# Optimization experiments

Hardware: AMD Instinct MI355X
Metric: run time of the kernel (lower is better)

Reference implementation:

```python
import jax, jax.numpy as jnp
import numpy as np

E = 64      # hidden_dim
FF = 128    # ff_dim
H = 4       # nhead
D = E // H  # head_dim = 16
STEPS = 16  # recursion_steps
IN = 200    # input_dim
B = 131072  # batch


def _ln(h, g, b):
    m = h.mean(-1, keepdims=True)
    v = ((h - m) ** 2).mean(-1, keepdims=True)
    return (h - m) * jax.lax.rsqrt(v + 1e-5) * g + b


def _ffn(h, w1, b1, w2, b2):
    return jax.nn.gelu(h @ w1.T + b1, approximate=False) @ w2.T + b2


def _forward(x, W_in, b_in, g_in, be_in,
             z_in_w, z_in_b, z_out_w, z_out_b,
             z_ffn_w1, z_ffn_b1, z_ffn_w2, z_ffn_b2,
             zn1_g, zn1_b, zn2_g, zn2_b,
             y_in_w, y_in_b, y_out_w, y_out_b,
             y_ffn_w1, y_ffn_b1, y_ffn_w2, y_ffn_b2,
             yn1_g, yn1_b, yn2_g, yn2_b,
             W_out, b_out):
    Bn = x.shape[0]
    x_proj = jax.nn.gelu(_ln(x @ W_in.T + b_in, g_in, be_in), approximate=False)  # [B,E]
    y0 = jnp.zeros((Bn, E), dtype=x.dtype)
    z0 = jnp.zeros((Bn, E), dtype=x.dtype)
    scale = 1.0 / np.sqrt(D).astype(np.float32)
    Wv_y = y_in_w[2 * E:]   # cross-attn over a single kv token: softmax weight == 1,
    bv_y = y_in_b[2 * E:]   # so output = out_proj(v_proj(z)) exactly (no approximation)

    def step(carry, _):
        y, z = carry
        seq = jnp.stack([x_proj, y, z], axis=1)            # [B,3,E]
        qkv = seq @ z_in_w.T + z_in_b                      # [B,3,3E]
        q, k, v = jnp.split(qkv, 3, axis=-1)
        rh = lambda t: t.reshape(Bn, 3, H, D).transpose(0, 2, 1, 3)  # [B,H,3,D]
        q, k, v = rh(q), rh(k), rh(v)
        att = jax.nn.softmax(jnp.einsum('bhsd,bhtd->bhst', q, k) * scale, axis=-1)
        o = jnp.einsum('bhst,bhtd->bhsd', att, v).transpose(0, 2, 1, 3).reshape(Bn, 3, E)
        o = o @ z_out_w.T + z_out_b
        z_res = _ln(z + o[:, 2, :], zn1_g, zn1_b)
        z2 = _ln(z_res + _ffn(z_res, z_ffn_w1, z_ffn_b1, z_ffn_w2, z_ffn_b2), zn2_g, zn2_b)
        ca = (z2 @ Wv_y.T + bv_y) @ y_out_w.T + y_out_b    # 1-token cross-attention
        y_res = _ln(y + ca, yn1_g, yn1_b)
        y2 = _ln(y_res + _ffn(y_res, y_ffn_w1, y_ffn_b1, y_ffn_w2, y_ffn_b2), yn2_g, yn2_b)
        return (y2, z2), None

    (y, z), _ = jax.lax.scan(step, (y0, z0), None, length=STEPS)
    return (y @ W_out.T + b_out)[:, 0]                     # [B]


def setup_inputs() -> dict:
    key = jax.random.key(0)
    ks = jax.random.split(key, 12)
    f = lambda k, s: jax.random.normal(k, s, dtype=jnp.float32) * 0.05
    zeros = lambda s: jnp.zeros(s, dtype=jnp.float32)
    ones = lambda s: jnp.ones(s, dtype=jnp.float32)
    return {
        'x': jax.random.normal(ks[0], (B, IN), dtype=jnp.float32),
        'W_in': f(ks[1], (E, IN)), 'b_in': zeros((E,)),
        'g_in': ones((E,)), 'be_in': zeros((E,)),
        'z_in_w': f(ks[2], (3 * E, E)), 'z_in_b': zeros((3 * E,)),
        'z_out_w': f(ks[3], (E, E)), 'z_out_b': zeros((E,)),
        'z_ffn_w1': f(ks[4], (FF, E)), 'z_ffn_b1': zeros((FF,)),
        'z_ffn_w2': f(ks[5], (E, FF)), 'z_ffn_b2': zeros((E,)),
        'zn1_g': ones((E,)), 'zn1_b': zeros((E,)),
        'zn2_g': ones((E,)), 'zn2_b': zeros((E,)),
        'y_in_w': f(ks[6], (3 * E, E)), 'y_in_b': zeros((3 * E,)),
        'y_out_w': f(ks[7], (E, E)), 'y_out_b': zeros((E,)),
        'y_ffn_w1': f(ks[8], (FF, E)), 'y_ffn_b1': zeros((FF,)),
        'y_ffn_w2': f(ks[9], (E, FF)), 'y_ffn_b2': zeros((E,)),
        'yn1_g': ones((E,)), 'yn1_b': zeros((E,)),
        'yn2_g': ones((E,)), 'yn2_b': zeros((E,)),
        'W_out': f(ks[10], (1, E)), 'b_out': zeros((1,)),
    }


def reference(x, W_in, b_in, g_in, be_in,
              z_in_w, z_in_b, z_out_w, z_out_b,
              z_ffn_w1, z_ffn_b1, z_ffn_w2, z_ffn_b2,
              zn1_g, zn1_b, zn2_g, zn2_b,
              y_in_w, y_in_b, y_out_w, y_out_b,
              y_ffn_w1, y_ffn_b1, y_ffn_w2, y_ffn_b2,
              yn1_g, yn1_b, yn2_g, yn2_b,
              W_out, b_out):
    return _forward(x, W_in, b_in, g_in, be_in,
                    z_in_w, z_in_b, z_out_w, z_out_b,
                    z_ffn_w1, z_ffn_b1, z_ffn_w2, z_ffn_b2,
                    zn1_g, zn1_b, zn2_g, zn2_b,
                    y_in_w, y_in_b, y_out_w, y_out_b,
                    y_ffn_w1, y_ffn_b1, y_ffn_w2, y_ffn_b2,
                    yn1_g, yn1_b, yn2_g, yn2_b,
                    W_out, b_out)
```

## Files before the change

### kernel.cpp

```cpp
#include <hip/hip_runtime.h>
#include <math.h>


constexpr int STEPS = 16;
constexpr int INDIM = 200;

typedef __attribute__((ext_vector_type(8))) short bfrag8;
typedef __attribute__((ext_vector_type(4))) float f32x4;
typedef __attribute__((ext_vector_type(4))) short s16x4;

constexpr int FB_WIN  = 0;
constexpr int NFRAG   = 140;
constexpr int NPARAM  = 1544;

constexpr int LB_ZQ   = 0;
constexpr int LB_ZK   = 8;
constexpr int LB_ZV   = 16;
constexpr int LB_ZOUT = 24;
constexpr int LB_ZF1  = 32;
constexpr int LB_ZF2  = 48;
constexpr int LB_YV   = 64;
constexpr int LB_YOUT = 72;
constexpr int LB_YF1  = 80;
constexpr int LB_YF2  = 96;
constexpr int NSTEADY = 112;

constexpr int PB_BIN   = 0;
constexpr int PB_GIN   = 64;
constexpr int PB_BEIN  = 128;
constexpr int PB_ZINB  = 192;
constexpr int PB_ZOUTB = 384;
constexpr int PB_ZF1B  = 448;
constexpr int PB_ZF2B  = 576;
constexpr int PB_ZN1G  = 640;
constexpr int PB_ZN1B  = 704;
constexpr int PB_ZN2G  = 768;
constexpr int PB_ZN2B  = 832;
constexpr int PB_YVB   = 896;
constexpr int PB_YOUTB = 960;
constexpr int PB_YF1B  = 1024;
constexpr int PB_YF2B  = 1152;
constexpr int PB_YN1G  = 1216;
constexpr int PB_YN1B  = 1280;
constexpr int PB_YN2G  = 1344;
constexpr int PB_YN2B  = 1408;
constexpr int PB_WOUT  = 1472;
constexpr int PB_BOUT  = 1536;

constexpr int S64      = 72;
constexpr int L_W      = 0;
constexpr int L_P      = 57344;
constexpr int L_ACT    = 60432;
constexpr int WAVE_SH  = 1152;
constexpr int NWAVE    = 16;
constexpr int ARENA_SH = L_ACT + NWAVE * WAVE_SH;

struct Params {
  const float *x, *W_in, *b_in, *g_in, *be_in;
  const float *z_in_w, *z_in_b, *z_out_w, *z_out_b;
  const float *z_ffn_w1, *z_ffn_b1, *z_ffn_w2, *z_ffn_b2;
  const float *zn1_g, *zn1_b, *zn2_g, *zn2_b;
  const float *y_in_w, *y_in_b, *y_out_w, *y_out_b;
  const float *y_ffn_w1, *y_ffn_b1, *y_ffn_w2, *y_ffn_b2;
  const float *yn1_g, *yn1_b, *yn2_g, *yn2_b;
  const float *W_out, *b_out;
  float *out;
  int nrows;
};

__device__ __forceinline__ ushort f2bf_rne(float f) {
  uint u = __float_as_uint(f);
  u += 0x7FFFu + ((u >> 16) & 1u);
  return (ushort)(u >> 16);
}

__device__ __forceinline__ ushort f2bf(float f) {
  return (ushort)((__float_as_uint(f) + 0x8000u) >> 16);
}
__device__ __forceinline__ uint pk2(float a, float b) {
  uint ua = __float_as_uint(a) + 0x8000u;
  uint ub = __float_as_uint(b) + 0x8000u;
  return (ua >> 16) | (ub & 0xFFFF0000u);
}
__device__ __forceinline__ float upk_lo(uint u) {
  return __uint_as_float(u << 16);
}
__device__ __forceinline__ float upk_hi(uint u) {
  return __uint_as_float(u & 0xFFFF0000u);
}
__device__ __forceinline__ f32x4 upk4(const uint* p) {
  f32x4 r;
  r.x = upk_lo(p[0]); r.y = upk_hi(p[0]);
  r.z = upk_lo(p[1]); r.w = upk_hi(p[1]);
  return r;
}
__device__ __forceinline__ float dot4(f32x4 a, f32x4 b) {
  return a.x * b.x + a.y * b.y + a.z * b.z + a.w * b.w;
}
__device__ __forceinline__ void stc(short* buf, int stride, int mt, int q,
                                    int s, f32x4 c) {
  s16x4 v;
  v.x = (short)f2bf(c.x); v.y = (short)f2bf(c.y);
  v.z = (short)f2bf(c.z); v.w = (short)f2bf(c.w);
  *(s16x4*)(buf + s * stride + mt * 16 + q * 4) = v;
}

__device__ __forceinline__ void c2b_p(const uint p[8], bfrag8& b0, bfrag8& b1,
                                      int lane) {
  const int srcA = (lane & 15) | ((lane & 16) << 1);
  const int srcB = srcA + 16;
  const bool odd = (lane & 32) != 0;
  uint ev0 = p[0], ev1 = p[1], ev2 = p[4], ev3 = p[5];
  uint od0 = p[2], od1 = p[3], od2 = p[6], od3 = p[7];
  uint rA0, rA1, rA2, rA3, rB0, rB1, rB2, rB3;
  {
    uint e, o;
    e = (uint)__shfl((int)ev0, srcA); o = (uint)__shfl((int)od0, srcA); rA0 = odd ? o : e;
    e = (uint)__shfl((int)ev1, srcA); o = (uint)__shfl((int)od1, srcA); rA1 = odd ? o : e;
    e = (uint)__shfl((int)ev2, srcA); o = (uint)__shfl((int)od2, srcA); rA2 = odd ? o : e;
    e = (uint)__shfl((int)ev3, srcA); o = (uint)__shfl((int)od3, srcA); rA3 = odd ? o : e;
    e = (uint)__shfl((int)ev0, srcB); o = (uint)__shfl((int)od0, srcB); rB0 = odd ? o : e;
    e = (uint)__shfl((int)ev1, srcB); o = (uint)__shfl((int)od1, srcB); rB1 = odd ? o : e;
    e = (uint)__shfl((int)ev2, srcB); o = (uint)__shfl((int)od2, srcB); rB2 = odd ? o : e;
    e = (uint)__shfl((int)ev3, srcB); o = (uint)__shfl((int)od3, srcB); rB3 = odd ? o : e;
  }
  union U { uint u[4]; bfrag8 b; };
  U u0, u1;
  u0.u[0] = rA0; u0.u[1] = rA1; u0.u[2] = rB0; u0.u[3] = rB1;
  u1.u[0] = rA2; u1.u[1] = rA3; u1.u[2] = rB2; u1.u[3] = rB3;
  b0 = u0.b; b1 = u1.b;
}
__device__ __forceinline__ void c2b(const f32x4 c[4], bfrag8& b0, bfrag8& b1,
                                    int lane) {
  uint p[8];
#pragma unroll
  for (int mt = 0; mt < 4; ++mt) {
    p[2 * mt]     = pk2(c[mt].x, c[mt].y);
    p[2 * mt + 1] = pk2(c[mt].z, c[mt].w);
  }
  c2b_p(p, b0, b1, lane);
}

template <int MT>
__device__ __forceinline__ void layerN(const short* in, const short* lw,
                                       int fbase, const float* bias, f32x4* c,
                                       int lane, int q, int s) {
  bfrag8 bf[2];
#pragma unroll
  for (int kt = 0; kt < 2; ++kt)
    bf[kt] = *(const bfrag8*)(in + s * S64 + kt * 32 + q * 8);
#pragma unroll
  for (int mt = 0; mt < MT; ++mt)
    c[mt] = *(const f32x4*)(bias + mt * 16 + q * 4);
#pragma unroll
  for (int mt = 0; mt < MT; ++mt) {
#pragma unroll
    for (int kt = 0; kt < 2; ++kt) {
      bfrag8 af = *(const bfrag8*)(lw + (fbase + mt * 2 + kt) * 512 + lane * 8);
      c[mt] = __builtin_amdgcn_mfma_f32_16x16x32_bf16(af, bf[kt], c[mt], 0, 0, 0);
    }
  }
}

template <int MT, int KT>
__device__ __forceinline__ void layerBK(const bfrag8* bf, const short* lw,
                                        int fbase, const float* bias, f32x4* c,
                                        int lane, int q) {
#pragma unroll
  for (int mt = 0; mt < MT; ++mt)
    c[mt] = *(const f32x4*)(bias + mt * 16 + q * 4);
#pragma unroll
  for (int mt = 0; mt < MT; ++mt) {
#pragma unroll
    for (int kt = 0; kt < KT; ++kt) {
      bfrag8 af = *(const bfrag8*)(lw + (fbase + mt * KT + kt) * 512 + lane * 8);
      c[mt] = __builtin_amdgcn_mfma_f32_16x16x32_bf16(af, bf[kt], c[mt], 0, 0, 0);
    }
  }
}

template <int MT>
__device__ __forceinline__ void layerB2(const bfrag8* bfA, const bfrag8* bfB,
                                        const short* lw, int fbase,
                                        const float* bias, f32x4* cA, f32x4* cB,
                                        int lane, int q) {
#pragma unroll
  for (int mt = 0; mt < MT; ++mt) {
    f32x4 b4 = *(const f32x4*)(bias + mt * 16 + q * 4);
    cA[mt] = b4; cB[mt] = b4;
  }
#pragma unroll
  for (int mt = 0; mt < MT; ++mt) {
#pragma unroll
    for (int kt = 0; kt < 2; ++kt) {
      bfrag8 af = *(const bfrag8*)(lw + (fbase + mt * 2 + kt) * 512 + lane * 8);
      cA[mt] = __builtin_amdgcn_mfma_f32_16x16x32_bf16(af, bfA[kt], cA[mt], 0, 0, 0);
      cB[mt] = __builtin_amdgcn_mfma_f32_16x16x32_bf16(af, bfB[kt], cB[mt], 0, 0, 0);
    }
  }
}

__device__ __forceinline__ void ffn2_via_th(const f32x4 h8[8], short* TH,
                                            const short* lw, int f2base,
                                            const float* b2, f32x4 c[4],
                                            int lane, int q, int s);

__device__ __forceinline__ void lnorm_c(f32x4 c[4], const float* g,
                                        const float* b, int q) {
  f32x4 s4 = (c[0] + c[1]) + (c[2] + c[3]);
  float sm = (s4.x + s4.y) + (s4.z + s4.w);
  sm += __shfl_xor(sm, 16); sm += __shfl_xor(sm, 32);
  float mean = sm * (1.f / 64.f);
  f32x4 vs4 = {0.f, 0.f, 0.f, 0.f};
#pragma unroll
  for (int mt = 0; mt < 4; ++mt) {
    f32x4 d = c[mt] - mean;
    c[mt] = d;
    vs4 = vs4 + d * d;
  }
  float vs = (vs4.x + vs4.y) + (vs4.z + vs4.w);
  vs += __shfl_xor(vs, 16); vs += __shfl_xor(vs, 32);
  float rs = rsqrtf(vs * (1.f / 64.f) + 1e-5f);
#pragma unroll
  for (int mt = 0; mt < 4; ++mt) {
    f32x4 g4 = *(const f32x4*)(g + mt * 16 + q * 4);
    f32x4 b4 = *(const f32x4*)(b + mt * 16 + q * 4);
    c[mt] = (c[mt] * rs) * g4 + b4;
  }
}

__device__ __forceinline__ f32x4 gelu4(f32x4 x) {
  const float K = 0.70710678118654752f;
  f32x4 ax;
  ax.x = fabsf(x.x) * K; ax.y = fabsf(x.y) * K;
  ax.z = fabsf(x.z) * K; ax.w = fabsf(x.w) * K;
  f32x4 u = ax * 0.47047f + 1.0f;
  f32x4 t;
  t.x = __builtin_amdgcn_rcpf(u.x); t.y = __builtin_amdgcn_rcpf(u.y);
  t.z = __builtin_amdgcn_rcpf(u.z); t.w = __builtin_amdgcn_rcpf(u.w);
  f32x4 poly = ((t * 0.7478556f + (-0.0958798f)) * t + 0.3480242f) * t;
  f32x4 gq = ax * ax;
  f32x4 e;
  e.x = __expf(-gq.x); e.y = __expf(-gq.y);
  e.z = __expf(-gq.z); e.w = __expf(-gq.w);
  f32x4 r = poly * e;
  f32x4 er;
  er.x = copysignf(1.0f - r.x, x.x); er.y = copysignf(1.0f - r.y, x.y);
  er.z = copysignf(1.0f - r.z, x.z); er.w = copysignf(1.0f - r.w, x.w);
  f32x4 h = x * 0.5f;
  return h + h * er;
}

__device__ __forceinline__ void ffn2_via_th(const f32x4 h8[8], short* TH,
                                            const short* lw, int f2base,
                                            const float* b2, f32x4 c[4],
                                            int lane, int q, int s) {
#pragma unroll
  for (int mt = 0; mt < 4; ++mt)
    c[mt] = *(const f32x4*)(b2 + mt * 16 + q * 4);
#pragma unroll
  for (int g = 0; g < 2; ++g) {
#pragma unroll
    for (int mt = 0; mt < 4; ++mt)
      stc(TH, S64, mt, q, s, gelu4(h8[4 * g + mt]));
    bfrag8 bf[2];
#pragma unroll
    for (int kt = 0; kt < 2; ++kt)
      bf[kt] = *(const bfrag8*)(TH + s * S64 + kt * 32 + q * 8);
#pragma unroll
    for (int mt = 0; mt < 4; ++mt) {
#pragma unroll
      for (int kt = 0; kt < 2; ++kt) {
        bfrag8 af =
            *(const bfrag8*)(lw + (f2base + mt * 4 + 2 * g + kt) * 512 + lane * 8);
        c[mt] = __builtin_amdgcn_mfma_f32_16x16x32_bf16(af, bf[kt], c[mt], 0, 0, 0);
      }
    }
  }
}

__global__ void prepack_kernel(Params p, ushort* wf) {
  int f = blockIdx.x;
  int lane = threadIdx.x;

  if (f == NFRAG) {
    float* pw = (float*)(wf + (size_t)NFRAG * 512);
    for (int t = lane; t < NPARAM; t += 64) {
      float v = 0.f;
      if      (t < 64)   v = p.b_in[t];
      else if (t < 128)  v = p.g_in[t - 64];
      else if (t < 192)  v = p.be_in[t - 128];
      else if (t < 384)  v = p.z_in_b[t - 192];
      else if (t < 448)  v = p.z_out_b[t - 384];
      else if (t < 576)  v = p.z_ffn_b1[t - 448];
      else if (t < 640)  v = p.z_ffn_b2[t - 576];
      else if (t < 704)  v = p.zn1_g[t - 640];
      else if (t < 768)  v = p.zn1_b[t - 704];
      else if (t < 832)  v = p.zn2_g[t - 768];
      else if (t < 896)  v = p.zn2_b[t - 832];
      else if (t < 960)  v = p.y_in_b[128 + t - 896];
      else if (t < 1024) v = p.y_out_b[t - 960];
      else if (t < 1152) v = p.y_ffn_b1[t - 1024];
      else if (t < 1216) v = p.y_ffn_b2[t - 1152];
      else if (t < 1280) v = p.yn1_g[t - 1216];
      else if (t < 1344) v = p.yn1_b[t - 1280];
      else if (t < 1408) v = p.yn2_g[t - 1344];
      else if (t < 1472) v = p.yn2_b[t - 1408];
      else if (t < 1536) v = p.W_out[t - 1472];
      else if (t == 1536) v = p.b_out[0];
      pw[t] = v;
    }
    return;
  }

  int q = lane >> 4, r = lane & 15;
  const float* src; int K, mt, kt, l;
  if (f < 28)        { src = p.W_in;                K = 200; mt = f / 7;  kt = f % 7; }
  else if (f < 36)   { l = f - 28;  src = p.z_in_w;            K = 64;  mt = l / 2; kt = l % 2; }
  else if (f < 44)   { l = f - 36;  src = p.z_in_w + 64 * 64;  K = 64;  mt = l / 2; kt = l % 2; }
  else if (f < 52)   { l = f - 44;  src = p.z_in_w + 128 * 64; K = 64;  mt = l / 2; kt = l % 2; }
  else if (f < 60)   { l = f - 52;  src = p.z_out_w;           K = 64;  mt = l / 2; kt = l % 2; }
  else if (f < 76)   { l = f - 60;  src = p.z_ffn_w1;          K = 64;  mt = l / 2; kt = l % 2; }
  else if (f < 92)   { l = f - 76;  src = p.z_ffn_w2;          K = 128; mt = l / 4; kt = l % 4; }
  else if (f < 100)  { l = f - 92;  src = p.y_in_w + 128 * 64; K = 64;  mt = l / 2; kt = l % 2; }
  else if (f < 108)  { l = f - 100; src = p.y_out_w;           K = 64;  mt = l / 2; kt = l % 2; }
  else if (f < 124)  { l = f - 108; src = p.y_ffn_w1;          K = 64;  mt = l / 2; kt = l % 2; }
  else               { l = f - 124; src = p.y_ffn_w2;          K = 128; mt = l / 4; kt = l % 4; }

  int row = mt * 16 + r;
  int col = kt * 32 + q * 8;
  bfrag8 o;
#pragma unroll
  for (int j = 0; j < 8; ++j) {
    int cc = col + j;
    float v = (cc < K) ? src[(size_t)row * K + cc] : 0.0f;
    o[j] = (short)f2bf_rne(v);
  }
  *(bfrag8*)(wf + (size_t)f * 512 + lane * 8) = o;
}

__global__ __launch_bounds__(1024, 1)
void trm_mfma_kernel(Params p, const ushort* wf) {
  __shared__ __align__(16) short arena[ARENA_SH];
  const int tid = threadIdx.x;
  const int wave = tid >> 6, lane = tid & 63;
  const int q = lane >> 4, s = lane & 15;

  {
    const uint4* srcw = (const uint4*)(wf + (size_t)28 * 512);
    uint4* dstw = (uint4*)(arena + L_W);
    for (int i = tid; i < NSTEADY * 64; i += 1024) dstw[i] = srcw[i];
    const uint4* srcp = (const uint4*)(wf + (size_t)NFRAG * 512);
    uint4* dstp = (uint4*)(arena + L_P);
    for (int i = tid; i < NPARAM / 4; i += 1024) dstp[i] = srcp[i];
  }
  __syncthreads();

  const short* LW = arena + L_W;
  const float* P  = (const float*)(arena + L_P);
  short* TH = arena + L_ACT + wave * WAVE_SH;

  const int chunks = (p.nrows + 255) / 256;
  for (int ic = blockIdx.x; ic < chunks; ic += gridDim.x) {
    const int row0 = ic * 256 + wave * 16;
    int row = row0 + s;
    if (row >= p.nrows) row = p.nrows - 1;

    bfrag8 xpB[2];
    {
      const float* xr = p.x + (size_t)row * INDIM;
      bfrag8 xb[7];
#pragma unroll
      for (int kt = 0; kt < 7; ++kt) {
        int k0i = kt * 32 + q * 8;
        bfrag8 t;
        if (kt < 6 || q == 0) {
          f32x4 lo = *(const f32x4*)(xr + k0i);
          f32x4 hi = *(const f32x4*)(xr + k0i + 4);
          t[0] = (short)f2bf(lo.x); t[1] = (short)f2bf(lo.y);
          t[2] = (short)f2bf(lo.z); t[3] = (short)f2bf(lo.w);
          t[4] = (short)f2bf(hi.x); t[5] = (short)f2bf(hi.y);
          t[6] = (short)f2bf(hi.z); t[7] = (short)f2bf(hi.w);
        } else {
#pragma unroll
          for (int j = 0; j < 8; ++j) t[j] = 0;
        }
        xb[kt] = t;
      }
      f32x4 c[4];
#pragma unroll
      for (int mt = 0; mt < 4; ++mt)
        c[mt] = *(const f32x4*)(P + PB_BIN + mt * 16 + q * 4);
#pragma unroll
      for (int mt = 0; mt < 4; ++mt)
#pragma unroll
        for (int kt = 0; kt < 7; ++kt) {
          bfrag8 af =
              *(const bfrag8*)(wf + (size_t)(FB_WIN + mt * 7 + kt) * 512 + lane * 8);
          c[mt] = __builtin_amdgcn_mfma_f32_16x16x32_bf16(af, xb[kt], c[mt], 0, 0, 0);
        }
      lnorm_c(c, P + PB_GIN, P + PB_BEIN, q);
#pragma unroll
      for (int mt = 0; mt < 4; ++mt) c[mt] = gelu4(c[mt]);
      c2b(c, xpB[0], xpB[1], lane);
    }

    uint k0p[8], v0p[8], zCp[8], yCp[8];
    bfrag8 zB[2], yB[2];
    {
      f32x4 ck[4], cv[4];
      layerBK<4, 2>(xpB, LW, LB_ZK, P + PB_ZINB + 64, ck, lane, q);
      layerBK<4, 2>(xpB, LW, LB_ZV, P + PB_ZINB + 128, cv, lane, q);
#pragma unroll
      for (int mt = 0; mt < 4; ++mt) {
        k0p[2 * mt]     = pk2(ck[mt].x, ck[mt].y);
        k0p[2 * mt + 1] = pk2(ck[mt].z, ck[mt].w);
        v0p[2 * mt]     = pk2(cv[mt].x, cv[mt].y);
        v0p[2 * mt + 1] = pk2(cv[mt].z, cv[mt].w);
        zCp[2 * mt] = 0u; zCp[2 * mt + 1] = 0u;
        yCp[2 * mt] = 0u; yCp[2 * mt + 1] = 0u;
      }
#pragma unroll
      for (int kt = 0; kt < 2; ++kt) {
        bfrag8 t;
#pragma unroll
        for (int j = 0; j < 8; ++j) t[j] = 0;
        zB[kt] = t; yB[kt] = t;
      }
    }

    for (int st = 0; st < STEPS; ++st) {
      float w0[4], w1[4], w2[4], wi[4];
      {
        f32x4 q2[4], kz[4], ky[4];
        layerBK<4, 2>(zB, LW, LB_ZQ, P + PB_ZINB, q2, lane, q);
        layerB2<4>(zB, yB, LW, LB_ZK, P + PB_ZINB + 64, kz, ky, lane, q);
#pragma unroll
        for (int mt = 0; mt < 4; ++mt) {
          float a0 = dot4(q2[mt], upk4(k0p + 2 * mt));
          float a1 = dot4(q2[mt], ky[mt]);
          float a2 = dot4(q2[mt], kz[mt]);
          a0 += __shfl_xor(a0, 16); a0 += __shfl_xor(a0, 32);
          a1 += __shfl_xor(a1, 16); a1 += __shfl_xor(a1, 32);
          a2 += __shfl_xor(a2, 16); a2 += __shfl_xor(a2, 32);
          a0 *= 0.25f; a1 *= 0.25f; a2 *= 0.25f;
          float mx = fmaxf(a0, fmaxf(a1, a2));
          float e0 = __expf(a0 - mx), e1 = __expf(a1 - mx), e2 = __expf(a2 - mx);
          w0[mt] = e0; w1[mt] = e1; w2[mt] = e2;
          wi[mt] = __builtin_amdgcn_rcpf(e0 + e1 + e2);
        }
      }
      {
        f32x4 vz[4], vy[4];
        layerB2<4>(zB, yB, LW, LB_ZV, P + PB_ZINB + 128, vz, vy, lane, q);
#pragma unroll
        for (int mt = 0; mt < 4; ++mt) {
          f32x4 v0 = upk4(v0p + 2 * mt);
          f32x4 o = (v0 * w0[mt] + vy[mt] * w1[mt] + vz[mt] * w2[mt]) * wi[mt];
          stc(TH, S64, mt, q, s, o);
        }
      }

      uint zrp[8];
      {
        f32x4 zr[4];
        layerN<4>(TH, LW, LB_ZOUT, P + PB_ZOUTB, zr, lane, q, s);
#pragma unroll
        for (int mt = 0; mt < 4; ++mt) zr[mt] = zr[mt] + upk4(zCp + 2 * mt);
        lnorm_c(zr, P + PB_ZN1G, P + PB_ZN1B, q);
#pragma unroll
        for (int mt = 0; mt < 4; ++mt) {
          stc(TH, S64, mt, q, s, zr[mt]);
          zrp[2 * mt]     = pk2(zr[mt].x, zr[mt].y);
          zrp[2 * mt + 1] = pk2(zr[mt].z, zr[mt].w);
        }
      }

      f32x4 z2[4];
      {
        f32x4 h8[8];
        layerN<8>(TH, LW, LB_ZF1, P + PB_ZF1B, h8, lane, q, s);
        ffn2_via_th(h8, TH, LW, LB_ZF2, P + PB_ZF2B, z2, lane, q, s);
      }
#pragma unroll
      for (int mt = 0; mt < 4; ++mt) z2[mt] = z2[mt] + upk4(zrp + 2 * mt);
      lnorm_c(z2, P + PB_ZN2G, P + PB_ZN2B, q);
      {
        uint zp[8];
#pragma unroll
        for (int mt = 0; mt < 4; ++mt) {
          zp[2 * mt]     = pk2(z2[mt].x, z2[mt].y);
          zp[2 * mt + 1] = pk2(z2[mt].z, z2[mt].w);
          zCp[2 * mt] = zp[2 * mt]; zCp[2 * mt + 1] = zp[2 * mt + 1];
        }
        c2b_p(zp, zB[0], zB[1], lane);
      }

      f32x4 t4[4];
      layerBK<4, 2>(zB, LW, LB_YV, P + PB_YVB, t4, lane, q);
#pragma unroll
      for (int mt = 0; mt < 4; ++mt) stc(TH, S64, mt, q, s, t4[mt]);

      uint yrp[8];
      {
        f32x4 yr[4];
        layerN<4>(TH, LW, LB_YOUT, P + PB_YOUTB, yr, lane, q, s);
#pragma unroll
        for (int mt = 0; mt < 4; ++mt) yr[mt] = yr[mt] + upk4(yCp + 2 * mt);
        lnorm_c(yr, P + PB_YN1G, P + PB_YN1B, q);
#pragma unroll
        for (int mt = 0; mt < 4; ++mt) {
          stc(TH, S64, mt, q, s, yr[mt]);
          yrp[2 * mt]     = pk2(yr[mt].x, yr[mt].y);
          yrp[2 * mt + 1] = pk2(yr[mt].z, yr[mt].w);
        }
      }

      f32x4 y2[4];
      {
        f32x4 h8[8];
        layerN<8>(TH, LW, LB_YF1, P + PB_YF1B, h8, lane, q, s);
        ffn2_via_th(h8, TH, LW, LB_YF2, P + PB_YF2B, y2, lane, q, s);
      }
#pragma unroll
      for (int mt = 0; mt < 4; ++mt) y2[mt] = y2[mt] + upk4(yrp + 2 * mt);
      lnorm_c(y2, P + PB_YN2G, P + PB_YN2B, q);
      {
        uint yp[8];
#pragma unroll
        for (int mt = 0; mt < 4; ++mt) {
          yp[2 * mt]     = pk2(y2[mt].x, y2[mt].y);
          yp[2 * mt + 1] = pk2(y2[mt].z, y2[mt].w);
          yCp[2 * mt] = yp[2 * mt]; yCp[2 * mt + 1] = yp[2 * mt + 1];
        }
        c2b_p(yp, yB[0], yB[1], lane);
      }
    }

    float acc = 0.f;
#pragma unroll
    for (int mt = 0; mt < 4; ++mt) {
      f32x4 w4 = *(const f32x4*)(P + PB_WOUT + mt * 16 + q * 4);
      acc += dot4(upk4(yCp + 2 * mt), w4);
    }
    acc += __shfl_xor(acc, 16); acc += __shfl_xor(acc, 32);
    if (q == 0 && (row0 + s) < p.nrows) p.out[row0 + s] = acc + P[PB_BOUT];
  }
}

extern "C" void kernel_launch(void* const* d_in, const int* in_sizes, int n_in,
                              void* d_out, int out_size, void* d_ws,
                              size_t ws_size, hipStream_t stream) {
  Params p;
  const float* const* in = (const float* const*)d_in;
  p.x        = in[0];  p.W_in     = in[1];  p.b_in     = in[2];
  p.g_in     = in[3];  p.be_in    = in[4];
  p.z_in_w   = in[5];  p.z_in_b   = in[6];
  p.z_out_w  = in[7];  p.z_out_b  = in[8];
  p.z_ffn_w1 = in[9];  p.z_ffn_b1 = in[10];
  p.z_ffn_w2 = in[11]; p.z_ffn_b2 = in[12];
  p.zn1_g    = in[13]; p.zn1_b    = in[14];
  p.zn2_g    = in[15]; p.zn2_b    = in[16];
  p.y_in_w   = in[17]; p.y_in_b   = in[18];
  p.y_out_w  = in[19]; p.y_out_b  = in[20];
  p.y_ffn_w1 = in[21]; p.y_ffn_b1 = in[22];
  p.y_ffn_w2 = in[23]; p.y_ffn_b2 = in[24];
  p.yn1_g    = in[25]; p.yn1_b    = in[26];
  p.yn2_g    = in[27]; p.yn2_b    = in[28];
  p.W_out    = in[29]; p.b_out    = in[30];
  p.out      = (float*)d_out;
  p.nrows    = in_sizes[0] / INDIM;

  if (ws_size < (size_t)NFRAG * 1024 + NPARAM * 4) return;
  ushort* wf = (ushort*)d_ws;

  hipLaunchKernelGGL(prepack_kernel, dim3(NFRAG + 1), dim3(64), 0, stream, p, wf);
  hipLaunchKernelGGL(trm_mfma_kernel, dim3(256), dim3(1024), 0, stream, p, wf);
}
```

Measured before the change: 838.3 us.

## Process two 16-row tiles per wave to reuse weight fragments across MFMAs

```diff
diff --git a/kernel.cpp b/kernel.cpp
--- a/kernel.cpp
+++ b/kernel.cpp
@@ -142,39 +142,28 @@
 }
 
 template <int MT>
-__device__ __forceinline__ void layerN(const short* in, const short* lw,
-                                       int fbase, const float* bias, f32x4* c,
-                                       int lane, int q, int s) {
-  bfrag8 bf[2];
-#pragma unroll
-  for (int kt = 0; kt < 2; ++kt)
-    bf[kt] = *(const bfrag8*)(in + s * S64 + kt * 32 + q * 8);
-#pragma unroll
-  for (int mt = 0; mt < MT; ++mt)
-    c[mt] = *(const f32x4*)(bias + mt * 16 + q * 4);
+__device__ __forceinline__ void layerN2(const short* in0, const short* in1,
+                                        const short* lw, int fbase,
+                                        const float* bias, f32x4* c0, f32x4* c1,
+                                        int lane, int q, int s) {
+  bfrag8 b0[2], b1[2];
+#pragma unroll
+  for (int kt = 0; kt < 2; ++kt) {
+    b0[kt] = *(const bfrag8*)(in0 + s * S64 + kt * 32 + q * 8);
+    b1[kt] = *(const bfrag8*)(in1 + s * S64 + kt * 32 + q * 8);
+  }
+#pragma unroll
+  for (int mt = 0; mt < MT; ++mt) {
+    f32x4 b4 = *(const f32x4*)(bias + mt * 16 + q * 4);
+    c0[mt] = b4; c1[mt] = b4;
+  }
 #pragma unroll
   for (int mt = 0; mt < MT; ++mt) {
 #pragma unroll
     for (int kt = 0; kt < 2; ++kt) {
       bfrag8 af = *(const bfrag8*)(lw + (fbase + mt * 2 + kt) * 512 + lane * 8);
-      c[mt] = __builtin_amdgcn_mfma_f32_16x16x32_bf16(af, bf[kt], c[mt], 0, 0, 0);
-    }
-  }
-}
-
-template <int MT, int KT>
-__device__ __forceinline__ void layerBK(const bfrag8* bf, const short* lw,
-                                        int fbase, const float* bias, f32x4* c,
-                                        int lane, int q) {
-#pragma unroll
-  for (int mt = 0; mt < MT; ++mt)
-    c[mt] = *(const f32x4*)(bias + mt * 16 + q * 4);
-#pragma unroll
-  for (int mt = 0; mt < MT; ++mt) {
-#pragma unroll
-    for (int kt = 0; kt < KT; ++kt) {
-      bfrag8 af = *(const bfrag8*)(lw + (fbase + mt * KT + kt) * 512 + lane * 8);
-      c[mt] = __builtin_amdgcn_mfma_f32_16x16x32_bf16(af, bf[kt], c[mt], 0, 0, 0);
+      c0[mt] = __builtin_amdgcn_mfma_f32_16x16x32_bf16(af, b0[kt], c0[mt], 0, 0, 0);
+      c1[mt] = __builtin_amdgcn_mfma_f32_16x16x32_bf16(af, b1[kt], c1[mt], 0, 0, 0);
     }
   }
 }
@@ -200,10 +189,29 @@
   }
 }
 
-__device__ __forceinline__ void ffn2_via_th(const f32x4 h8[8], short* TH,
-                                            const short* lw, int f2base,
-                                            const float* b2, f32x4 c[4],
-                                            int lane, int q, int s);
+template <int MT>
+__device__ __forceinline__ void layerB4(const bfrag8* bf0, const bfrag8* bf1,
+                                        const bfrag8* bf2, const bfrag8* bf3,
+                                        const short* lw, int fbase,
+                                        const float* bias, f32x4* c0, f32x4* c1,
+                                        f32x4* c2, f32x4* c3, int lane, int q) {
+#pragma unroll
+  for (int mt = 0; mt < MT; ++mt) {
+    f32x4 b4 = *(const f32x4*)(bias + mt * 16 + q * 4);
+    c0[mt] = b4; c1[mt] = b4; c2[mt] = b4; c3[mt] = b4;
+  }
+#pragma unroll
+  for (int mt = 0; mt < MT; ++mt) {
+#pragma unroll
+    for (int kt = 0; kt < 2; ++kt) {
+      bfrag8 af = *(const bfrag8*)(lw + (fbase + mt * 2 + kt) * 512 + lane * 8);
+      c0[mt] = __builtin_amdgcn_mfma_f32_16x16x32_bf16(af, bf0[kt], c0[mt], 0, 0, 0);
+      c1[mt] = __builtin_amdgcn_mfma_f32_16x16x32_bf16(af, bf1[kt], c1[mt], 0, 0, 0);
+      c2[mt] = __builtin_amdgcn_mfma_f32_16x16x32_bf16(af, bf2[kt], c2[mt], 0, 0, 0);
+      c3[mt] = __builtin_amdgcn_mfma_f32_16x16x32_bf16(af, bf3[kt], c3[mt], 0, 0, 0);
+    }
+  }
+}
 
 __device__ __forceinline__ void lnorm_c(f32x4 c[4], const float* g,
                                         const float* b, int q) {
@@ -251,29 +259,37 @@
   return h + h * er;
 }
 
-__device__ __forceinline__ void ffn2_via_th(const f32x4 h8[8], short* TH,
-                                            const short* lw, int f2base,
-                                            const float* b2, f32x4 c[4],
-                                            int lane, int q, int s) {
-#pragma unroll
-  for (int mt = 0; mt < 4; ++mt)
-    c[mt] = *(const f32x4*)(b2 + mt * 16 + q * 4);
+__device__ __forceinline__ void ffn2_via_th2(const f32x4 h0[8], const f32x4 h1[8],
+                                             short* TH0, short* TH1,
+                                             const short* lw, int f2base,
+                                             const float* b2, f32x4 c0[4],
+                                             f32x4 c1[4], int lane, int q, int s) {
+#pragma unroll
+  for (int mt = 0; mt < 4; ++mt) {
+    f32x4 b4 = *(const f32x4*)(b2 + mt * 16 + q * 4);
+    c0[mt] = b4; c1[mt] = b4;
+  }
 #pragma unroll
   for (int g = 0; g < 2; ++g) {
 #pragma unroll
-    for (int mt = 0; mt < 4; ++mt)
-      stc(TH, S64, mt, q, s, gelu4(h8[4 * g + mt]));
-    bfrag8 bf[2];
-#pragma unroll
-    for (int kt = 0; kt < 2; ++kt)
-      bf[kt] = *(const bfrag8*)(TH + s * S64 + kt * 32 + q * 8);
+    for (int mt = 0; mt < 4; ++mt) {
+      stc(TH0, S64, mt, q, s, gelu4(h0[4 * g + mt]));
+      stc(TH1, S64, mt, q, s, gelu4(h1[4 * g + mt]));
+    }
+    bfrag8 bf0[2], bf1[2];
+#pragma unroll
+    for (int kt = 0; kt < 2; ++kt) {
+      bf0[kt] = *(const bfrag8*)(TH0 + s * S64 + kt * 32 + q * 8);
+      bf1[kt] = *(const bfrag8*)(TH1 + s * S64 + kt * 32 + q * 8);
+    }
 #pragma unroll
     for (int mt = 0; mt < 4; ++mt) {
 #pragma unroll
       for (int kt = 0; kt < 2; ++kt) {
         bfrag8 af =
             *(const bfrag8*)(lw + (f2base + mt * 4 + 2 * g + kt) * 512 + lane * 8);
-        c[mt] = __builtin_amdgcn_mfma_f32_16x16x32_bf16(af, bf[kt], c[mt], 0, 0, 0);
+        c0[mt] = __builtin_amdgcn_mfma_f32_16x16x32_bf16(af, bf0[kt], c0[mt], 0, 0, 0);
+        c1[mt] = __builtin_amdgcn_mfma_f32_16x16x32_bf16(af, bf1[kt], c1[mt], 0, 0, 0);
       }
     }
   }
@@ -339,7 +355,7 @@
   *(bfrag8*)(wf + (size_t)f * 512 + lane * 8) = o;
 }
 
-__global__ __launch_bounds__(1024, 1)
+__global__ __launch_bounds__(512, 1)
 void trm_mfma_kernel(Params p, const ushort* wf) {
   __shared__ __align__(16) short arena[ARENA_SH];
   const int tid = threadIdx.x;
@@ -349,202 +365,257 @@
   {
     const uint4* srcw = (const uint4*)(wf + (size_t)28 * 512);
     uint4* dstw = (uint4*)(arena + L_W);
-    for (int i = tid; i < NSTEADY * 64; i += 1024) dstw[i] = srcw[i];
+    for (int i = tid; i < NSTEADY * 64; i += 512) dstw[i] = srcw[i];
     const uint4* srcp = (const uint4*)(wf + (size_t)NFRAG * 512);
     uint4* dstp = (uint4*)(arena + L_P);
-    for (int i = tid; i < NPARAM / 4; i += 1024) dstp[i] = srcp[i];
+    for (int i = tid; i < NPARAM / 4; i += 512) dstp[i] = srcp[i];
   }
   __syncthreads();
 
   const short* LW = arena + L_W;
   const float* P  = (const float*)(arena + L_P);
-  short* TH = arena + L_ACT + wave * WAVE_SH;
+  short* TH0 = arena + L_ACT + (2 * wave) * WAVE_SH;
+  short* TH1 = TH0 + WAVE_SH;
 
   const int chunks = (p.nrows + 255) / 256;
   for (int ic = blockIdx.x; ic < chunks; ic += gridDim.x) {
-    const int row0 = ic * 256 + wave * 16;
-    int row = row0 + s;
-    if (row >= p.nrows) row = p.nrows - 1;
-
-    bfrag8 xpB[2];
+    int rw[2];
+#pragma unroll
+    for (int t = 0; t < 2; ++t) {
+      int r = ic * 256 + wave * 16 + t * 128 + s;
+      rw[t] = (r < p.nrows) ? r : (p.nrows - 1);
+    }
+
+    bfrag8 xpB[2][2];
     {
-      const float* xr = p.x + (size_t)row * INDIM;
-      bfrag8 xb[7];
-#pragma unroll
-      for (int kt = 0; kt < 7; ++kt) {
-        int k0i = kt * 32 + q * 8;
-        bfrag8 t;
-        if (kt < 6 || q == 0) {
-          f32x4 lo = *(const f32x4*)(xr + k0i);
-          f32x4 hi = *(const f32x4*)(xr + k0i + 4);
-          t[0] = (short)f2bf(lo.x); t[1] = (short)f2bf(lo.y);
-          t[2] = (short)f2bf(lo.z); t[3] = (short)f2bf(lo.w);
-          t[4] = (short)f2bf(hi.x); t[5] = (short)f2bf(hi.y);
-          t[6] = (short)f2bf(hi.z); t[7] = (short)f2bf(hi.w);
-        } else {
-#pragma unroll
-          for (int j = 0; j < 8; ++j) t[j] = 0;
-        }
-        xb[kt] = t;
-      }
-      f32x4 c[4];
-#pragma unroll
-      for (int mt = 0; mt < 4; ++mt)
-        c[mt] = *(const f32x4*)(P + PB_BIN + mt * 16 + q * 4);
+      bfrag8 xb[2][7];
+#pragma unroll
+      for (int t = 0; t < 2; ++t) {
+        const float* xr = p.x + (size_t)rw[t] * INDIM;
+#pragma unroll
+        for (int kt = 0; kt < 7; ++kt) {
+          int k0i = kt * 32 + q * 8;
+          bfrag8 v;
+          if (kt < 6 || q == 0) {
+            f32x4 lo = *(const f32x4*)(xr + k0i);
+            f32x4 hi = *(const f32x4*)(xr + k0i + 4);
+            v[0] = (short)f2bf(lo.x); v[1] = (short)f2bf(lo.y);
+            v[2] = (short)f2bf(lo.z); v[3] = (short)f2bf(lo.w);
+            v[4] = (short)f2bf(hi.x); v[5] = (short)f2bf(hi.y);
+            v[6] = (short)f2bf(hi.z); v[7] = (short)f2bf(hi.w);
+          } else {
+#pragma unroll
+            for (int j = 0; j < 8; ++j) v[j] = 0;
+          }
+          xb[t][kt] = v;
+        }
+      }
+      f32x4 c[2][4];
+#pragma unroll
+      for (int mt = 0; mt < 4; ++mt) {
+        f32x4 b4 = *(const f32x4*)(P + PB_BIN + mt * 16 + q * 4);
+        c[0][mt] = b4; c[1][mt] = b4;
+      }
 #pragma unroll
       for (int mt = 0; mt < 4; ++mt)
 #pragma unroll
         for (int kt = 0; kt < 7; ++kt) {
           bfrag8 af =
               *(const bfrag8*)(wf + (size_t)(FB_WIN + mt * 7 + kt) * 512 + lane * 8);
-          c[mt] = __builtin_amdgcn_mfma_f32_16x16x32_bf16(af, xb[kt], c[mt], 0, 0, 0);
-        }
-      lnorm_c(c, P + PB_GIN, P + PB_BEIN, q);
-#pragma unroll
-      for (int mt = 0; mt < 4; ++mt) c[mt] = gelu4(c[mt]);
-      c2b(c, xpB[0], xpB[1], lane);
-    }
-
-    uint k0p[8], v0p[8], zCp[8], yCp[8];
-    bfrag8 zB[2], yB[2];
+          c[0][mt] = __builtin_amdgcn_mfma_f32_16x16x32_bf16(af, xb[0][kt], c[0][mt], 0, 0, 0);
+          c[1][mt] = __builtin_amdgcn_mfma_f32_16x16x32_bf16(af, xb[1][kt], c[1][mt], 0, 0, 0);
+        }
+#pragma unroll
+      for (int t = 0; t < 2; ++t) {
+        lnorm_c(c[t], P + PB_GIN, P + PB_BEIN, q);
+#pragma unroll
+        for (int mt = 0; mt < 4; ++mt) c[t][mt] = gelu4(c[t][mt]);
+        c2b(c[t], xpB[t][0], xpB[t][1], lane);
+      }
+    }
+
+    uint k0p[2][8], v0p[2][8], zCp[2][8], yCp[2][8];
+    bfrag8 zB[2][2], yB[2][2];
     {
-      f32x4 ck[4], cv[4];
-      layerBK<4, 2>(xpB, LW, LB_ZK, P + PB_ZINB + 64, ck, lane, q);
-      layerBK<4, 2>(xpB, LW, LB_ZV, P + PB_ZINB + 128, cv, lane, q);
+      f32x4 ck[2][4], cv[2][4];
+      layerB2<4>(xpB[0], xpB[1], LW, LB_ZK, P + PB_ZINB + 64, ck[0], ck[1], lane, q);
+      layerB2<4>(xpB[0], xpB[1], LW, LB_ZV, P + PB_ZINB + 128, cv[0], cv[1], lane, q);
+#pragma unroll
+      for (int t = 0; t < 2; ++t) {
+#pragma unroll
+        for (int mt = 0; mt < 4; ++mt) {
+          k0p[t][2 * mt]     = pk2(ck[t][mt].x, ck[t][mt].y);
+          k0p[t][2 * mt + 1] = pk2(ck[t][mt].z, ck[t][mt].w);
+          v0p[t][2 * mt]     = pk2(cv[t][mt].x, cv[t][mt].y);
+          v0p[t][2 * mt + 1] = pk2(cv[t][mt].z, cv[t][mt].w);
+          zCp[t][2 * mt] = 0u; zCp[t][2 * mt + 1] = 0u;
+          yCp[t][2 * mt] = 0u; yCp[t][2 * mt + 1] = 0u;
+        }
+#pragma unroll
+        for (int kt = 0; kt < 2; ++kt) {
+          bfrag8 zr0;
+#pragma unroll
+          for (int j = 0; j < 8; ++j) zr0[j] = 0;
+          zB[t][kt] = zr0; yB[t][kt] = zr0;
+        }
+      }
+    }
+
+    for (int st = 0; st < STEPS; ++st) {
+      float w0[2][4], w1[2][4], w2[2][4], wi[2][4];
+      {
+        f32x4 q2[2][4], kz[2][4], ky[2][4];
+        layerB2<4>(zB[0], zB[1], LW, LB_ZQ, P + PB_ZINB, q2[0], q2[1], lane, q);
+        layerB4<4>(zB[0], yB[0], zB[1], yB[1], LW, LB_ZK, P + PB_ZINB + 64,
+                   kz[0], ky[0], kz[1], ky[1], lane, q);
+#pragma unroll
+        for (int t = 0; t < 2; ++t) {
+#pragma unroll
+          for (int mt = 0; mt < 4; ++mt) {
+            float a0 = dot4(q2[t][mt], upk4(k0p[t] + 2 * mt));
+            float a1 = dot4(q2[t][mt], ky[t][mt]);
+            float a2 = dot4(q2[t][mt], kz[t][mt]);
+            a0 += __shfl_xor(a0, 16); a0 += __shfl_xor(a0, 32);
+            a1 += __shfl_xor(a1, 16); a1 += __shfl_xor(a1, 32);
+            a2 += __shfl_xor(a2, 16); a2 += __shfl_xor(a2, 32);
+            a0 *= 0.25f; a1 *= 0.25f; a2 *= 0.25f;
+            float mx = fmaxf(a0, fmaxf(a1, a2));
+            float e0 = __expf(a0 - mx), e1 = __expf(a1 - mx), e2 = __expf(a2 - mx);
+            w0[t][mt] = e0; w1[t][mt] = e1; w2[t][mt] = e2;
+            wi[t][mt] = __builtin_amdgcn_rcpf(e0 + e1 + e2);
+          }
+        }
+      }
+      {
+        f32x4 vz[2][4], vy[2][4];
+        layerB4<4>(zB[0], yB[0], zB[1], yB[1], LW, LB_ZV, P + PB_ZINB + 128,
+                   vz[0], vy[0], vz[1], vy[1], lane, q);
+#pragma unroll
+        for (int mt = 0; mt < 4; ++mt) {
+          f32x4 o0 = (upk4(v0p[0] + 2 * mt) * w0[0][mt] + vy[0][mt] * w1[0][mt] +
+                      vz[0][mt] * w2[0][mt]) * wi[0][mt];
+          stc(TH0, S64, mt, q, s, o0);
+          f32x4 o1 = (upk4(v0p[1] + 2 * mt) * w0[1][mt] + vy[1][mt] * w1[1][mt] +
+                      vz[1][mt] * w2[1][mt]) * wi[1][mt];
+          stc(TH1, S64, mt, q, s, o1);
+        }
+      }
+
+      uint zrp[2][8];
+      {
+        f32x4 zr[2][4];
+        layerN2<4>(TH0, TH1, LW, LB_ZOUT, P + PB_ZOUTB, zr[0], zr[1], lane, q, s);
+#pragma unroll
+        for (int t = 0; t < 2; ++t) {
+#pragma unroll
+          for (int mt = 0; mt < 4; ++mt) zr[t][mt] = zr[t][mt] + upk4(zCp[t] + 2 * mt);
+          lnorm_c(zr[t], P + PB_ZN1G, P + PB_ZN1B, q);
+        }
+#pragma unroll
+        for (int mt = 0; mt < 4; ++mt) {
+          stc(TH0, S64, mt, q, s, zr[0][mt]);
+          stc(TH1, S64, mt, q, s, zr[1][mt]);
+        }
+#pragma unroll
+        for (int t = 0; t < 2; ++t)
+#pragma unroll
+          for (int mt = 0; mt < 4; ++mt) {
+            zrp[t][2 * mt]     = pk2(zr[t][mt].x, zr[t][mt].y);
+            zrp[t][2 * mt + 1] = pk2(zr[t][mt].z, zr[t][mt].w);
+          }
+      }
+
+      f32x4 z2[2][4];
+      {
+        f32x4 h8[2][8];
+        layerN2<8>(TH0, TH1, LW, LB_ZF1, P + PB_ZF1B, h8[0], h8[1], lane, q, s);
+        ffn2_via_th2(h8[0], h8[1], TH0, TH1, LW, LB_ZF2, P + PB_ZF2B,
+                     z2[0], z2[1], lane, q, s);
+      }
+#pragma unroll
+      for (int t = 0; t < 2; ++t) {
+#pragma unroll
+        for (int mt = 0; mt < 4; ++mt) z2[t][mt] = z2[t][mt] + upk4(zrp[t] + 2 * mt);
+        lnorm_c(z2[t], P + PB_ZN2G, P + PB_ZN2B, q);
+        uint zp[8];
+#pragma unroll
+        for (int mt = 0; mt < 4; ++mt) {
+          zp[2 * mt]     = pk2(z2[t][mt].x, z2[t][mt].y);
+          zp[2 * mt + 1] = pk2(z2[t][mt].z, z2[t][mt].w);
+          zCp[t][2 * mt] = zp[2 * mt]; zCp[t][2 * mt + 1] = zp[2 * mt + 1];
+        }
+        c2b_p(zp, zB[t][0], zB[t][1], lane);
+      }
+
+      {
+        f32x4 t4[2][4];
+        layerB2<4>(zB[0], zB[1], LW, LB_YV, P + PB_YVB, t4[0], t4[1], lane, q);
+#pragma unroll
+        for (int mt = 0; mt < 4; ++mt) {
+          stc(TH0, S64, mt, q, s, t4[0][mt]);
+          stc(TH1, S64, mt, q, s, t4[1][mt]);
+        }
+      }
+
+      uint yrp[2][8];
+      {
+        f32x4 yr[2][4];
+        layerN2<4>(TH0, TH1, LW, LB_YOUT, P + PB_YOUTB, yr[0], yr[1], lane, q, s);
+#pragma unroll
+        for (int t = 0; t < 2; ++t) {
+#pragma unroll
+          for (int mt = 0; mt < 4; ++mt) yr[t][mt] = yr[t][mt] + upk4(yCp[t] + 2 * mt);
+          lnorm_c(yr[t], P + PB_YN1G, P + PB_YN1B, q);
+        }
+#pragma unroll
+        for (int mt = 0; mt < 4; ++mt) {
+          stc(TH0, S64, mt, q, s, yr[0][mt]);
+          stc(TH1, S64, mt, q, s, yr[1][mt]);
+        }
+#pragma unroll
+        for (int t = 0; t < 2; ++t)
+#pragma unroll
+          for (int mt = 0; mt < 4; ++mt) {
+            yrp[t][2 * mt]     = pk2(yr[t][mt].x, yr[t][mt].y);
+            yrp[t][2 * mt + 1] = pk2(yr[t][mt].z, yr[t][mt].w);
+          }
+      }
+
+      f32x4 y2[2][4];
+      {
+        f32x4 h8[2][8];
+        layerN2<8>(TH0, TH1, LW, LB_YF1, P + PB_YF1B, h8[0], h8[1], lane, q, s);
+        ffn2_via_th2(h8[0], h8[1], TH0, TH1, LW, LB_YF2, P + PB_YF2B,
+                     y2[0], y2[1], lane, q, s);
+      }
+#pragma unroll
+      for (int t = 0; t < 2; ++t) {
+#pragma unroll
+        for (int mt = 0; mt < 4; ++mt) y2[t][mt] = y2[t][mt] + upk4(yrp[t] + 2 * mt);
+        lnorm_c(y2[t], P + PB_YN2G, P + PB_YN2B, q);
+        uint yp[8];
+#pragma unroll
+        for (int mt = 0; mt < 4; ++mt) {
+          yp[2 * mt]     = pk2(y2[t][mt].x, y2[t][mt].y);
+          yp[2 * mt + 1] = pk2(y2[t][mt].z, y2[t][mt].w);
+          yCp[t][2 * mt] = yp[2 * mt]; yCp[t][2 * mt + 1] = yp[2 * mt + 1];
+        }
+        c2b_p(yp, yB[t][0], yB[t][1], lane);
+      }
+    }
+
+#pragma unroll
+    for (int t = 0; t < 2; ++t) {
+      float acc = 0.f;
 #pragma unroll
       for (int mt = 0; mt < 4; ++mt) {
-        k0p[2 * mt]     = pk2(ck[mt].x, ck[mt].y);
-        k0p[2 * mt + 1] = pk2(ck[mt].z, ck[mt].w);
-        v0p[2 * mt]     = pk2(cv[mt].x, cv[mt].y);
-        v0p[2 * mt + 1] = pk2(cv[mt].z, cv[mt].w);
-        zCp[2 * mt] = 0u; zCp[2 * mt + 1] = 0u;
-        yCp[2 * mt] = 0u; yCp[2 * mt + 1] = 0u;
-      }
-#pragma unroll
-      for (int kt = 0; kt < 2; ++kt) {
-        bfrag8 t;
-#pragma unroll
-        for (int j = 0; j < 8; ++j) t[j] = 0;
-        zB[kt] = t; yB[kt] = t;
-      }
-    }
-
-    for (int st = 0; st < STEPS; ++st) {
-      float w0[4], w1[4], w2[4], wi[4];
-      {
-        f32x4 q2[4], kz[4], ky[4];
-        layerBK<4, 2>(zB, LW, LB_ZQ, P + PB_ZINB, q2, lane, q);
-        layerB2<4>(zB, yB, LW, LB_ZK, P + PB_ZINB + 64, kz, ky, lane, q);
-#pragma unroll
-        for (int mt = 0; mt < 4; ++mt) {
-          float a0 = dot4(q2[mt], upk4(k0p + 2 * mt));
-          float a1 = dot4(q2[mt], ky[mt]);
-          float a2 = dot4(q2[mt], kz[mt]);
-          a0 += __shfl_xor(a0, 16); a0 += __shfl_xor(a0, 32);
-          a1 += __shfl_xor(a1, 16); a1 += __shfl_xor(a1, 32);
-          a2 += __shfl_xor(a2, 16); a2 += __shfl_xor(a2, 32);
-          a0 *= 0.25f; a1 *= 0.25f; a2 *= 0.25f;
-          float mx = fmaxf(a0, fmaxf(a1, a2));
-          float e0 = __expf(a0 - mx), e1 = __expf(a1 - mx), e2 = __expf(a2 - mx);
-          w0[mt] = e0; w1[mt] = e1; w2[mt] = e2;
-          wi[mt] = __builtin_amdgcn_rcpf(e0 + e1 + e2);
-        }
-      }
-      {
-        f32x4 vz[4], vy[4];
-        layerB2<4>(zB, yB, LW, LB_ZV, P + PB_ZINB + 128, vz, vy, lane, q);
-#pragma unroll
-        for (int mt = 0; mt < 4; ++mt) {
-          f32x4 v0 = upk4(v0p + 2 * mt);
-          f32x4 o = (v0 * w0[mt] + vy[mt] * w1[mt] + vz[mt] * w2[mt]) * wi[mt];
-          stc(TH, S64, mt, q, s, o);
-        }
-      }
-
-      uint zrp[8];
-      {
-        f32x4 zr[4];
-        layerN<4>(TH, LW, LB_ZOUT, P + PB_ZOUTB, zr, lane, q, s);
-#pragma unroll
-        for (int mt = 0; mt < 4; ++mt) zr[mt] = zr[mt] + upk4(zCp + 2 * mt);
-        lnorm_c(zr, P + PB_ZN1G, P + PB_ZN1B, q);
-#pragma unroll
-        for (int mt = 0; mt < 4; ++mt) {
-          stc(TH, S64, mt, q, s, zr[mt]);
-          zrp[2 * mt]     = pk2(zr[mt].x, zr[mt].y);
-          zrp[2 * mt + 1] = pk2(zr[mt].z, zr[mt].w);
-        }
-      }
-
-      f32x4 z2[4];
-      {
-        f32x4 h8[8];
-        layerN<8>(TH, LW, LB_ZF1, P + PB_ZF1B, h8, lane, q, s);
-        ffn2_via_th(h8, TH, LW, LB_ZF2, P + PB_ZF2B, z2, lane, q, s);
-      }
-#pragma unroll
-      for (int mt = 0; mt < 4; ++mt) z2[mt] = z2[mt] + upk4(zrp + 2 * mt);
-      lnorm_c(z2, P + PB_ZN2G, P + PB_ZN2B, q);
-      {
-        uint zp[8];
-#pragma unroll
-        for (int mt = 0; mt < 4; ++mt) {
-          zp[2 * mt]     = pk2(z2[mt].x, z2[mt].y);
-          zp[2 * mt + 1] = pk2(z2[mt].z, z2[mt].w);
-          zCp[2 * mt] = zp[2 * mt]; zCp[2 * mt + 1] = zp[2 * mt + 1];
-        }
-        c2b_p(zp, zB[0], zB[1], lane);
-      }
-
-      f32x4 t4[4];
-      layerBK<4, 2>(zB, LW, LB_YV, P + PB_YVB, t4, lane, q);
-#pragma unroll
-      for (int mt = 0; mt < 4; ++mt) stc(TH, S64, mt, q, s, t4[mt]);
-
-      uint yrp[8];
-      {
-        f32x4 yr[4];
-        layerN<4>(TH, LW, LB_YOUT, P + PB_YOUTB, yr, lane, q, s);
-#pragma unroll
-        for (int mt = 0; mt < 4; ++mt) yr[mt] = yr[mt] + upk4(yCp + 2 * mt);
-        lnorm_c(yr, P + PB_YN1G, P + PB_YN1B, q);
-#pragma unroll
-        for (int mt = 0; mt < 4; ++mt) {
-          stc(TH, S64, mt, q, s, yr[mt]);
-          yrp[2 * mt]     = pk2(yr[mt].x, yr[mt].y);
-          yrp[2 * mt + 1] = pk2(yr[mt].z, yr[mt].w);
-        }
-      }
-
-      f32x4 y2[4];
-      {
-        f32x4 h8[8];
-        layerN<8>(TH, LW, LB_YF1, P + PB_YF1B, h8, lane, q, s);
-        ffn2_via_th(h8, TH, LW, LB_YF2, P + PB_YF2B, y2, lane, q, s);
-      }
-#pragma unroll
-      for (int mt = 0; mt < 4; ++mt) y2[mt] = y2[mt] + upk4(yrp + 2 * mt);
-      lnorm_c(y2, P + PB_YN2G, P + PB_YN2B, q);
-      {
-        uint yp[8];
-#pragma unroll
-        for (int mt = 0; mt < 4; ++mt) {
-          yp[2 * mt]     = pk2(y2[mt].x, y2[mt].y);
-          yp[2 * mt + 1] = pk2(y2[mt].z, y2[mt].w);
-          yCp[2 * mt] = yp[2 * mt]; yCp[2 * mt + 1] = yp[2 * mt + 1];
-        }
-        c2b_p(yp, yB[0], yB[1], lane);
-      }
-    }
-
-    float acc = 0.f;
-#pragma unroll
-    for (int mt = 0; mt < 4; ++mt) {
-      f32x4 w4 = *(const f32x4*)(P + PB_WOUT + mt * 16 + q * 4);
-      acc += dot4(upk4(yCp + 2 * mt), w4);
-    }
-    acc += __shfl_xor(acc, 16); acc += __shfl_xor(acc, 32);
-    if (q == 0 && (row0 + s) < p.nrows) p.out[row0 + s] = acc + P[PB_BOUT];
+        f32x4 w4 = *(const f32x4*)(P + PB_WOUT + mt * 16 + q * 4);
+        acc += dot4(upk4(yCp[t] + 2 * mt), w4);
+      }
+      acc += __shfl_xor(acc, 16); acc += __shfl_xor(acc, 32);
+      int orow = ic * 256 + wave * 16 + t * 128 + s;
+      if (q == 0 && orow < p.nrows) p.out[orow] = acc + P[PB_BOUT];
+    }
   }
 }
 
@@ -575,5 +646,5 @@
   ushort* wf = (ushort*)d_ws;
 
   hipLaunchKernelGGL(prepack_kernel, dim3(NFRAG + 1), dim3(64), 0, stream, p, wf);
-  hipLaunchKernelGGL(trm_mfma_kernel, dim3(256), dim3(1024), 0, stream, p, wf);
-}
+  hipLaunchKernelGGL(trm_mfma_kernel, dim3(256), dim3(512), 0, stream, p, wf);
+}
```

Result: slower. 876.3 us (+4.5%).
